# Performance work log

Hardware: AMD Instinct MI355X
Metric: run time of the kernel (lower is better)

## Reference

```python
import jax, jax.numpy as jnp
import numpy as np

N_NODES = 100000
N_EDGES = 1600000
D_FEAT = 64
COS_EPS = 1e-8  # torch.nn.functional.cosine_similarity default eps


def setup_inputs() -> dict:
    key = jax.random.key(0)
    k1, k2 = jax.random.split(key)
    features = jax.random.normal(k1, (N_NODES, D_FEAT), dtype=jnp.float32)
    edge_index = jax.random.randint(k2, (2, N_EDGES), 0, N_NODES, dtype=jnp.int64)
    return {"features": features, "edge_index": edge_index}


def _mean_agg(h, src, dst, n_nodes):
    # copy_u: message = h[src]; fn.mean: per-dst mean over incoming messages
    msg_sum = jax.ops.segment_sum(h[src], dst, num_segments=n_nodes)  # [N, d]
    deg = jax.ops.segment_sum(jnp.ones(src.shape, h.dtype), dst, num_segments=n_nodes)  # [N]
    deg = deg[:, None]
    # nodes with zero in-degree get 0 (DGL mean semantics)
    return jnp.where(deg > 0, msg_sum / jnp.maximum(deg, 1.0), 0.0)


def reference(features, edge_index):
    src, dst = edge_index[0], edge_index[1]
    n = features.shape[0]
    x1 = _mean_agg(features, src, dst, n)   # gcn1
    x2 = _mean_agg(x1, src, dst, n)         # gcn2
    # cosine similarity along feature dim
    dot = jnp.sum(x1 * x2, axis=-1)
    n1 = jnp.linalg.norm(x1, axis=-1)
    n2 = jnp.linalg.norm(x2, axis=-1)
    cos = dot / jnp.maximum(n1 * n2, COS_EPS)
    w = cos[:, None]
    return w * x2 + (1.0 - w) * x1
```

## Files before the change

kernel.cpp:

```cpp
#include <hip/hip_runtime.h>
#include <hip/hip_fp16.h>
#include <math.h>

#define N_NODES 100000
#define N_EDGES 1600000
#define D_FEAT  64

#define NPB     256
#define NBC     ((N_NODES + NPB - 1) / NPB)
#define HIST_WGS 256
#define NV4     (N_EDGES / 4)
#define CHUNK4  ((NV4 + HIST_WGS - 1) / HIST_WGS)
#define RAW_CAP 5120
#define CASTN   ((N_NODES * D_FEAT) / 4)

#define CAST1   2250
#define CAST2   1000
#define CAST3   750
#define CAST4   750
#define CO1     0
#define CO2     (CAST1 * 256)
#define CO3     (CO2 + CAST2 * 256)
#define CO4     (CO3 + CAST3 * 512)

#define GCAP    68


__device__ __forceinline__ void cast_slice(const float* __restrict__ feat,
                                           __half* __restrict__ feat_h, int i) {
    if (i < CASTN) {
        float4 v = ((const float4*)feat)[i];
        __half2 h0 = __floats2half2_rn(v.x, v.y);
        __half2 h1 = __floats2half2_rn(v.z, v.w);
        uint2 st;
        st.x = *(unsigned*)&h0;
        st.y = *(unsigned*)&h1;
        ((uint2*)feat_h)[i] = st;
    }
}

__device__ __forceinline__ uint4 pack8(const float* v) {
    __half2 h0 = __floats2half2_rn(v[0], v[1]);
    __half2 h1 = __floats2half2_rn(v[2], v[3]);
    __half2 h2 = __floats2half2_rn(v[4], v[5]);
    __half2 h3 = __floats2half2_rn(v[6], v[7]);
    uint4 st;
    st.x = *(unsigned*)&h0; st.y = *(unsigned*)&h1;
    st.z = *(unsigned*)&h2; st.w = *(unsigned*)&h3;
    return st;
}

__device__ __forceinline__ void unp8(uint4 u, float* a) {
    { __half2 h = *(__half2*)&u.x; float2 f = __half22float2(h); a[0]=f.x; a[1]=f.y; }
    { __half2 h = *(__half2*)&u.y; float2 f = __half22float2(h); a[2]=f.x; a[3]=f.y; }
    { __half2 h = *(__half2*)&u.z; float2 f = __half22float2(h); a[4]=f.x; a[5]=f.y; }
    { __half2 h = *(__half2*)&u.w; float2 f = __half22float2(h); a[6]=f.x; a[7]=f.y; }
}

__device__ __forceinline__ void acc4(uint4 u, __half2& h0, __half2& h1,
                                     __half2& h2, __half2& h3) {
    h0 = __hadd2(h0, *(__half2*)&u.x);
    h1 = __hadd2(h1, *(__half2*)&u.y);
    h2 = __hadd2(h2, *(__half2*)&u.z);
    h3 = __hadd2(h3, *(__half2*)&u.w);
}

__device__ __forceinline__ int block_excl_scan_512(int v, int t, int* wsum) {
    int lane = t & 63, wv = t >> 6;
    int incl = v;
    #pragma unroll
    for (int m = 1; m < 64; m <<= 1) {
        int o = __shfl_up(incl, m);
        if (lane >= m) incl += o;
    }
    if (lane == 63) wsum[wv] = incl;
    __syncthreads();
    int prefix = 0;
    #pragma unroll
    for (int j = 0; j < 8; j++)
        if (j < wv) prefix += wsum[j];
    return prefix + incl - v;
}

__device__ __forceinline__ int block_excl_scan_256(int v, int t, int* wsum) {
    int lane = t & 63, wv = t >> 6;
    int incl = v;
    #pragma unroll
    for (int m = 1; m < 64; m <<= 1) {
        int o = __shfl_up(incl, m);
        if (lane >= m) incl += o;
    }
    if (lane == 63) wsum[wv] = incl;
    __syncthreads();
    int prefix = 0;
    #pragma unroll
    for (int j = 0; j < 4; j++)
        if (j < wv) prefix += wsum[j];
    return prefix + incl - v;
}


__global__ __launch_bounds__(256) void k1_hist_cast(
        const float* __restrict__ feat,
        __half* __restrict__ feat_h,
        const int4* __restrict__ dst4,
        int* __restrict__ percnt) {
    if (blockIdx.x >= HIST_WGS) {
        cast_slice(feat, feat_h, CO1 + (blockIdx.x - HIST_WGS) * 256 + threadIdx.x);
        return;
    }
    __shared__ int cnt[NBC];
    int wg = blockIdx.x, t = threadIdx.x;
    for (int i = t; i < NBC; i += 256) cnt[i] = 0;
    __syncthreads();
    int i0 = wg * CHUNK4;
    int i1 = min(i0 + CHUNK4, NV4);
    for (int i = i0 + t; i < i1; i += 256) {
        int4 d = dst4[i];
        atomicAdd(&cnt[d.x >> 8], 1);
        atomicAdd(&cnt[d.y >> 8], 1);
        atomicAdd(&cnt[d.z >> 8], 1);
        atomicAdd(&cnt[d.w >> 8], 1);
    }
    __syncthreads();
    for (int i = t; i < NBC; i += 256)
        percnt[wg * NBC + i] = cnt[i];
}


__global__ __launch_bounds__(256) void k2_colscan(
        const int* __restrict__ percnt,
        int* __restrict__ pexcl,
        int* __restrict__ bhist,
        const float* __restrict__ feat,
        __half* __restrict__ feat_h) {
    if (blockIdx.x >= NBC) {
        cast_slice(feat, feat_h, CO2 + (blockIdx.x - NBC) * 256 + threadIdx.x);
        return;
    }
    __shared__ int wsum[4];
    int b = blockIdx.x, t = threadIdx.x;
    int v = percnt[t * NBC + b];
    int excl = block_excl_scan_256(v, t, wsum);
    pexcl[b * HIST_WGS + t] = excl;
    if (t == HIST_WGS - 1) bhist[b] = excl + v;
}


__global__ __launch_bounds__(512) void k3_bucketize(
        const int4* __restrict__ src4,
        const int4* __restrict__ dst4,
        const int* __restrict__ bhist,
        const int* __restrict__ pexcl,
        unsigned int* __restrict__ tmp1,
        const float* __restrict__ feat,
        __half* __restrict__ feat_h) {
    if (blockIdx.x >= HIST_WGS) {
        cast_slice(feat, feat_h, CO3 + (blockIdx.x - HIST_WGS) * 512 + threadIdx.x);
        return;
    }
    __shared__ int base[NBC];
    __shared__ int cur[NBC];
    __shared__ int wsum[8];
    int wg = blockIdx.x, t = threadIdx.x;
    int v = (t < NBC) ? bhist[t] : 0;
    int excl = block_excl_scan_512(v, t, wsum);
    if (t < NBC) {
        base[t] = excl + pexcl[t * HIST_WGS + wg];
        cur[t] = 0;
    }
    __syncthreads();
    int i0 = wg * CHUNK4;
    int i1 = min(i0 + CHUNK4, NV4);
    for (int i = i0 + t; i < i1; i += 512) {
        int4 d = dst4[i];
        int4 s = src4[i];
        {
            int b = d.x >> 8; int r = atomicAdd(&cur[b], 1);
            tmp1[base[b] + r] = ((unsigned)s.x << 8) | (unsigned)(d.x & 255);
        }
        {
            int b = d.y >> 8; int r = atomicAdd(&cur[b], 1);
            tmp1[base[b] + r] = ((unsigned)s.y << 8) | (unsigned)(d.y & 255);
        }
        {
            int b = d.z >> 8; int r = atomicAdd(&cur[b], 1);
            tmp1[base[b] + r] = ((unsigned)s.z << 8) | (unsigned)(d.z & 255);
        }
        {
            int b = d.w >> 8; int r = atomicAdd(&cur[b], 1);
            tmp1[base[b] + r] = ((unsigned)s.w << 8) | (unsigned)(d.w & 255);
        }
    }
}


__global__ __launch_bounds__(512) void k4_bucket_csr(
        const unsigned int* __restrict__ tmp1,
        const int* __restrict__ bhist,
        int* __restrict__ offsets,
        int* __restrict__ csr_src,
        const float* __restrict__ feat,
        __half* __restrict__ feat_h) {
    if (blockIdx.x >= NBC) {
        cast_slice(feat, feat_h, CO4 + (blockIdx.x - NBC) * 512 + threadIdx.x);
        return;
    }
    __shared__ int cnt[NPB];
    __shared__ int off[NPB];
    __shared__ int wsum[8];
    __shared__ int buf[RAW_CAP];
    __shared__ int sEbase, sEcnt;
    int b = blockIdx.x, t = threadIdx.x;

    {
        int v = (t < NBC) ? bhist[t] : 0;
        int ex = block_excl_scan_512(v, t, wsum);
        if (t == b) { sEbase = ex; sEcnt = v; }
    }
    if (t < NPB) cnt[t] = 0;
    __syncthreads();
    int ebase = sEbase;
    int ecnt  = sEcnt;
    int node0 = b * NPB;

    if (ecnt <= RAW_CAP) {
        unsigned myv[10];
        #pragma unroll
        for (int k = 0; k < 10; k++) {
            int i = t + k * 512;
            if (i < ecnt) {
                unsigned u = tmp1[ebase + i];
                myv[k] = u;
                atomicAdd(&cnt[u & 255], 1);
            }
        }
        __syncthreads();

        int v = (t < NPB) ? cnt[t] : 0;
        int excl = block_excl_scan_512(v, t, wsum);
        if (t < NPB) {
            off[t] = excl;
            cnt[t] = 0;
            if (node0 + t < N_NODES) offsets[node0 + t] = ebase + excl;
        }
        if (b == NBC - 1 && t == 0) offsets[N_NODES] = N_EDGES;
        __syncthreads();

        #pragma unroll
        for (int k = 0; k < 10; k++) {
            int i = t + k * 512;
            if (i < ecnt) {
                unsigned u = myv[k];
                int d = (int)(u & 255);
                int r = atomicAdd(&cnt[d], 1);
                buf[off[d] + r] = (int)(u >> 8);
            }
        }
        __syncthreads();
        for (int i = t; i < ecnt; i += 512)
            csr_src[ebase + i] = buf[i];
    } else {
        for (int i = t; i < ecnt; i += 512)
            atomicAdd(&cnt[tmp1[ebase + i] & 255], 1);
        __syncthreads();

        int v = (t < NPB) ? cnt[t] : 0;
        int excl = block_excl_scan_512(v, t, wsum);
        if (t < NPB) {
            off[t] = excl;
            cnt[t] = 0;
            if (node0 + t < N_NODES) offsets[node0 + t] = ebase + excl;
        }
        if (b == NBC - 1 && t == 0) offsets[N_NODES] = N_EDGES;
        __syncthreads();

        for (int i = t; i < ecnt; i += 512) {
            unsigned u = tmp1[ebase + i];
            int d = (int)(u & 255);
            int r = atomicAdd(&cnt[d], 1);
            csr_src[ebase + off[d] + r] = (int)(u >> 8);
        }
    }
}


__global__ __launch_bounds__(256) void gather1_kernel(
        const __half* __restrict__ feat_h,
        const int* __restrict__ offsets,
        const int* __restrict__ csr,
        __half* __restrict__ x1_h) {
    __shared__ int snbr[4][8][GCAP];
    int wv   = threadIdx.x >> 6;
    int lane = threadIdx.x & 63;
    int g    = lane >> 3;
    int fl   = lane & 7;
    int node = (blockIdx.x * 4 + wv) * 8 + g;

    int base = offsets[node];
    int deg  = offsets[node + 1] - base;
    int dcap = min(deg, GCAP);

    int* my = snbr[wv][g];
    for (int j = fl; j < dcap; j += 8)
        my[j] = csr[base + j];
    __builtin_amdgcn_wave_barrier();

    __half2 a0 = __float2half2_rn(0.f), a1 = a0, a2 = a0, a3 = a0;
    __half2 b0 = a0, b1 = a0, b2 = a0, b3 = a0;
    const __half* fb = feat_h + (fl << 3);
    int j = 0;
    for (; j + 4 <= dcap; j += 4) {
        int4 s = *(const int4*)&my[j];
        uint4 u0 = *(const uint4*)(fb + ((size_t)s.x << 6));
        uint4 u1 = *(const uint4*)(fb + ((size_t)s.y << 6));
        uint4 u2 = *(const uint4*)(fb + ((size_t)s.z << 6));
        uint4 u3 = *(const uint4*)(fb + ((size_t)s.w << 6));
        acc4(u0, a0, a1, a2, a3);
        acc4(u1, b0, b1, b2, b3);
        acc4(u2, a0, a1, a2, a3);
        acc4(u3, b0, b1, b2, b3);
    }
    for (; j < dcap; ++j) {
        int s = my[j];
        uint4 u = *(const uint4*)(fb + ((size_t)s << 6));
        acc4(u, a0, a1, a2, a3);
    }
    for (j = GCAP; j < deg; ++j) {
        int s = csr[base + j];
        uint4 u = *(const uint4*)(fb + ((size_t)s << 6));
        acc4(u, a0, a1, a2, a3);
    }
    a0 = __hadd2(a0, b0); a1 = __hadd2(a1, b1);
    a2 = __hadd2(a2, b2); a3 = __hadd2(a3, b3);

    float invf = (deg > 0) ? __builtin_amdgcn_rcpf((float)deg) : 0.0f;
    float r[8];
    { float2 f = __half22float2(a0); r[0]=f.x*invf; r[1]=f.y*invf; }
    { float2 f = __half22float2(a1); r[2]=f.x*invf; r[3]=f.y*invf; }
    { float2 f = __half22float2(a2); r[4]=f.x*invf; r[5]=f.y*invf; }
    { float2 f = __half22float2(a3); r[6]=f.x*invf; r[7]=f.y*invf; }
    *(uint4*)(x1_h + ((size_t)node << 6) + (fl << 3)) = pack8(r);
}

__global__ __launch_bounds__(256) void gather2_finalize_kernel(
        const __half* __restrict__ x1_h,
        const int* __restrict__ offsets,
        const int* __restrict__ csr,
        float* __restrict__ out) {
    __shared__ int snbr[4][8][GCAP];
    int wv   = threadIdx.x >> 6;
    int lane = threadIdx.x & 63;
    int g    = lane >> 3;
    int fl   = lane & 7;
    int node = (blockIdx.x * 4 + wv) * 8 + g;

    int base = offsets[node];
    int deg  = offsets[node + 1] - base;
    int dcap = min(deg, GCAP);

    int* my = snbr[wv][g];
    for (int j = fl; j < dcap; j += 8)
        my[j] = csr[base + j];
    __builtin_amdgcn_wave_barrier();

    __half2 a0 = __float2half2_rn(0.f), a1 = a0, a2 = a0, a3 = a0;
    __half2 c0 = a0, c1 = a0, c2 = a0, c3 = a0;
    const __half* fb = x1_h + (fl << 3);
    int j = 0;
    for (; j + 4 <= dcap; j += 4) {
        int4 s = *(const int4*)&my[j];
        uint4 u0 = *(const uint4*)(fb + ((size_t)s.x << 6));
        uint4 u1 = *(const uint4*)(fb + ((size_t)s.y << 6));
        uint4 u2 = *(const uint4*)(fb + ((size_t)s.z << 6));
        uint4 u3 = *(const uint4*)(fb + ((size_t)s.w << 6));
        acc4(u0, a0, a1, a2, a3);
        acc4(u1, c0, c1, c2, c3);
        acc4(u2, a0, a1, a2, a3);
        acc4(u3, c0, c1, c2, c3);
    }
    for (; j < dcap; ++j) {
        int s = my[j];
        uint4 u = *(const uint4*)(fb + ((size_t)s << 6));
        acc4(u, a0, a1, a2, a3);
    }
    for (j = GCAP; j < deg; ++j) {
        int s = csr[base + j];
        uint4 u = *(const uint4*)(fb + ((size_t)s << 6));
        acc4(u, a0, a1, a2, a3);
    }
    a0 = __hadd2(a0, c0); a1 = __hadd2(a1, c1);
    a2 = __hadd2(a2, c2); a3 = __hadd2(a3, c3);

    float invf = (deg > 0) ? __builtin_amdgcn_rcpf((float)deg) : 0.0f;
    float b[8];
    { float2 f = __half22float2(a0); b[0]=f.x*invf; b[1]=f.y*invf; }
    { float2 f = __half22float2(a1); b[2]=f.x*invf; b[3]=f.y*invf; }
    { float2 f = __half22float2(a2); b[4]=f.x*invf; b[5]=f.y*invf; }
    { float2 f = __half22float2(a3); b[6]=f.x*invf; b[7]=f.y*invf; }

    float a[8];
    uint4 ua = *(const uint4*)(x1_h + ((size_t)node << 6) + (fl << 3));
    unp8(ua, a);

    float dot = 0.f, nn1 = 0.f, nn2 = 0.f;
    #pragma unroll
    for (int t = 0; t < 8; t++) {
        dot += a[t] * b[t];
        nn1 += a[t] * a[t];
        nn2 += b[t] * b[t];
    }
    #pragma unroll
    for (int m = 1; m < 8; m <<= 1) {
        dot += __shfl_xor(dot, m);
        nn1 += __shfl_xor(nn1, m);
        nn2 += __shfl_xor(nn2, m);
    }

    float denom = fmaxf(__builtin_amdgcn_sqrtf(nn1 * nn2), 1e-8f);
    float w = dot * __builtin_amdgcn_rcpf(denom);
    float omw = 1.0f - w;

    float4 r0, r1;
    r0.x = w*b[0] + omw*a[0]; r0.y = w*b[1] + omw*a[1];
    r0.z = w*b[2] + omw*a[2]; r0.w = w*b[3] + omw*a[3];
    r1.x = w*b[4] + omw*a[4]; r1.y = w*b[5] + omw*a[5];
    r1.z = w*b[6] + omw*a[6]; r1.w = w*b[7] + omw*a[7];
    float* po = out + ((size_t)node << 6) + (fl << 3);
    *(float4*)po = r0;
    *(float4*)(po + 4) = r1;
}


extern "C" void kernel_launch(void* const* d_in, const int* in_sizes, int n_in,
                              void* d_out, int out_size, void* d_ws, size_t ws_size,
                              hipStream_t stream) {
    const float* feat = (const float*)d_in[0];
    const int*   eidx = (const int*)d_in[1];
    const int4*  src4 = (const int4*)eidx;
    const int4*  dst4 = (const int4*)(eidx + N_EDGES);

    __half*       feat_h  = (__half*)d_ws;
    __half*       x1_h    = feat_h + (size_t)N_NODES * D_FEAT;
    unsigned int* tmp1    = (unsigned int*)(x1_h + (size_t)N_NODES * D_FEAT);
    int*          csr_src = (int*)(tmp1 + N_EDGES);
    int*          offsets = csr_src + N_EDGES;
    int*          percnt  = offsets + (N_NODES + 1);
    int*          pexcl   = percnt + HIST_WGS * NBC;
    int*          bhist   = pexcl + NBC * HIST_WGS;
    float*        out     = (float*)d_out;

    k1_hist_cast <<<HIST_WGS + CAST1, 256, 0, stream>>>(feat, feat_h, dst4, percnt);
    k2_colscan   <<<NBC + CAST2,      256, 0, stream>>>(percnt, pexcl, bhist, feat, feat_h);
    k3_bucketize <<<HIST_WGS + CAST3, 512, 0, stream>>>(src4, dst4, bhist, pexcl, tmp1, feat, feat_h);
    k4_bucket_csr<<<NBC + CAST4,      512, 0, stream>>>(tmp1, bhist, offsets, csr_src, feat, feat_h);

    int nblocks = N_NODES / 32;
    gather1_kernel<<<nblocks, 256, 0, stream>>>(feat_h, offsets, csr_src, x1_h);
    gather2_finalize_kernel<<<nblocks, 256, 0, stream>>>(x1_h, offsets, csr_src, out);
}
```

Measured before the change: 160.0 us.

## Merge CSR build phases into one cooperative kernel with grid syncs

Replaces the four separate preprocessing kernels (histogram, column scan, bucketize, per-bucket CSR) with a single cooperative kernel that separates the phases with grid.sync(). The fp32-to-fp16 feature cast is spread over the spare blocks during the histogram and bucketize phases. The aim is to remove kernel launch gaps and drain tails between phases. In exchange it depends on all 391 blocks being resident at once and pays for grid-wide barriers. A fallback multi-kernel path runs if the cooperative launch fails, and the overflow branch for buckets larger than the shared buffer was dropped.

```diff
diff --git a/kernel.cpp b/kernel.cpp
--- a/kernel.cpp
+++ b/kernel.cpp
@@ -1,6 +1,9 @@
 #include <hip/hip_runtime.h>
+#include <hip/hip_cooperative_groups.h>
 #include <hip/hip_fp16.h>
 #include <math.h>
+
+namespace cg = cooperative_groups;
 
 #define N_NODES 100000
 #define N_EDGES 1600000
@@ -13,15 +16,12 @@
 #define CHUNK4  ((NV4 + HIST_WGS - 1) / HIST_WGS)
 #define RAW_CAP 5120
 #define CASTN   ((N_NODES * D_FEAT) / 4)
-
-#define CAST1   2250
-#define CAST2   1000
-#define CAST3   750
-#define CAST4   750
-#define CO1     0
-#define CO2     (CAST1 * 256)
-#define CO3     (CO2 + CAST2 * 256)
-#define CO4     (CO3 + CAST3 * 512)
+#define GRID_PRE NBC
+
+#define CAST_BLKS  (GRID_PRE - HIST_WGS)
+#define CAST_ITERS 12
+
+#define SMEM_INTS 5640
 
 #define GCAP    68
 
@@ -39,6 +39,15 @@
     }
 }
 
+__device__ __forceinline__ void cast_batch(const float* __restrict__ feat,
+                                           __half* __restrict__ feat_h,
+                                           int batch, int blk, int t) {
+    #pragma unroll
+    for (int it = 0; it < CAST_ITERS; ++it)
+        cast_slice(feat, feat_h,
+                   ((batch * CAST_BLKS + blk) * CAST_ITERS + it) * 512 + t);
+}
+
 __device__ __forceinline__ uint4 pack8(const float* v) {
     __half2 h0 = __floats2half2_rn(v[0], v[1]);
     __half2 h1 = __floats2half2_rn(v[2], v[3]);
@@ -82,40 +91,16 @@
     return prefix + incl - v;
 }
 
-__device__ __forceinline__ int block_excl_scan_256(int v, int t, int* wsum) {
-    int lane = t & 63, wv = t >> 6;
-    int incl = v;
-    #pragma unroll
-    for (int m = 1; m < 64; m <<= 1) {
-        int o = __shfl_up(incl, m);
-        if (lane >= m) incl += o;
-    }
-    if (lane == 63) wsum[wv] = incl;
-    __syncthreads();
-    int prefix = 0;
-    #pragma unroll
-    for (int j = 0; j < 4; j++)
-        if (j < wv) prefix += wsum[j];
-    return prefix + incl - v;
-}
-
-
-__global__ __launch_bounds__(256) void k1_hist_cast(
-        const float* __restrict__ feat,
-        __half* __restrict__ feat_h,
-        const int4* __restrict__ dst4,
-        int* __restrict__ percnt) {
-    if (blockIdx.x >= HIST_WGS) {
-        cast_slice(feat, feat_h, CO1 + (blockIdx.x - HIST_WGS) * 256 + threadIdx.x);
-        return;
-    }
-    __shared__ int cnt[NBC];
-    int wg = blockIdx.x, t = threadIdx.x;
-    for (int i = t; i < NBC; i += 256) cnt[i] = 0;
-    __syncthreads();
-    int i0 = wg * CHUNK4;
+
+__device__ void phase_hist(int b, int t, int* smem,
+                           const int4* __restrict__ dst4,
+                           int* __restrict__ percnt) {
+    int* cnt = smem;
+    for (int i = t; i < NBC; i += 512) cnt[i] = 0;
+    __syncthreads();
+    int i0 = b * CHUNK4;
     int i1 = min(i0 + CHUNK4, NV4);
-    for (int i = i0 + t; i < i1; i += 256) {
+    for (int i = i0 + t; i < i1; i += 512) {
         int4 d = dst4[i];
         atomicAdd(&cnt[d.x >> 8], 1);
         atomicAdd(&cnt[d.y >> 8], 1);
@@ -123,165 +108,183 @@
         atomicAdd(&cnt[d.w >> 8], 1);
     }
     __syncthreads();
-    for (int i = t; i < NBC; i += 256)
-        percnt[wg * NBC + i] = cnt[i];
-}
-
-
-__global__ __launch_bounds__(256) void k2_colscan(
-        const int* __restrict__ percnt,
-        int* __restrict__ pexcl,
-        int* __restrict__ bhist,
-        const float* __restrict__ feat,
-        __half* __restrict__ feat_h) {
-    if (blockIdx.x >= NBC) {
-        cast_slice(feat, feat_h, CO2 + (blockIdx.x - NBC) * 256 + threadIdx.x);
-        return;
-    }
-    __shared__ int wsum[4];
-    int b = blockIdx.x, t = threadIdx.x;
-    int v = percnt[t * NBC + b];
-    int excl = block_excl_scan_256(v, t, wsum);
-    pexcl[b * HIST_WGS + t] = excl;
+    for (int i = t; i < NBC; i += 512)
+        percnt[b * NBC + i] = cnt[i];
+}
+
+__device__ void phase_colscan(int b, int t, int* smem,
+                              const int* __restrict__ percnt,
+                              int* __restrict__ pexcl,
+                              int* __restrict__ bhist) {
+    int* wsum = smem;
+    int v = (t < HIST_WGS) ? percnt[t * NBC + b] : 0;
+    int excl = block_excl_scan_512(v, t, wsum);
+    if (t < HIST_WGS) pexcl[b * HIST_WGS + t] = excl;
     if (t == HIST_WGS - 1) bhist[b] = excl + v;
 }
 
-
-__global__ __launch_bounds__(512) void k3_bucketize(
-        const int4* __restrict__ src4,
-        const int4* __restrict__ dst4,
-        const int* __restrict__ bhist,
-        const int* __restrict__ pexcl,
-        unsigned int* __restrict__ tmp1,
-        const float* __restrict__ feat,
-        __half* __restrict__ feat_h) {
-    if (blockIdx.x >= HIST_WGS) {
-        cast_slice(feat, feat_h, CO3 + (blockIdx.x - HIST_WGS) * 512 + threadIdx.x);
-        return;
-    }
-    __shared__ int base[NBC];
-    __shared__ int cur[NBC];
-    __shared__ int wsum[8];
-    int wg = blockIdx.x, t = threadIdx.x;
+__device__ void phase_bucketize(int b, int t, int* smem,
+                                const int4* __restrict__ src4,
+                                const int4* __restrict__ dst4,
+                                const int* __restrict__ bhist,
+                                const int* __restrict__ pexcl,
+                                unsigned int* __restrict__ tmp1) {
+    int* base = smem;
+    int* cur  = smem + NBC;
+    int* wsum = smem + 2 * NBC;
     int v = (t < NBC) ? bhist[t] : 0;
     int excl = block_excl_scan_512(v, t, wsum);
     if (t < NBC) {
-        base[t] = excl + pexcl[t * HIST_WGS + wg];
+        base[t] = excl + pexcl[t * HIST_WGS + b];
         cur[t] = 0;
     }
     __syncthreads();
-    int i0 = wg * CHUNK4;
+    int i0 = b * CHUNK4;
     int i1 = min(i0 + CHUNK4, NV4);
     for (int i = i0 + t; i < i1; i += 512) {
         int4 d = dst4[i];
         int4 s = src4[i];
         {
-            int b = d.x >> 8; int r = atomicAdd(&cur[b], 1);
-            tmp1[base[b] + r] = ((unsigned)s.x << 8) | (unsigned)(d.x & 255);
+            int bb = d.x >> 8; int r = atomicAdd(&cur[bb], 1);
+            tmp1[base[bb] + r] = ((unsigned)s.x << 8) | (unsigned)(d.x & 255);
         }
         {
-            int b = d.y >> 8; int r = atomicAdd(&cur[b], 1);
-            tmp1[base[b] + r] = ((unsigned)s.y << 8) | (unsigned)(d.y & 255);
+            int bb = d.y >> 8; int r = atomicAdd(&cur[bb], 1);
+            tmp1[base[bb] + r] = ((unsigned)s.y << 8) | (unsigned)(d.y & 255);
         }
         {
-            int b = d.z >> 8; int r = atomicAdd(&cur[b], 1);
-            tmp1[base[b] + r] = ((unsigned)s.z << 8) | (unsigned)(d.z & 255);
+            int bb = d.z >> 8; int r = atomicAdd(&cur[bb], 1);
+            tmp1[base[bb] + r] = ((unsigned)s.z << 8) | (unsigned)(d.z & 255);
         }
         {
-            int b = d.w >> 8; int r = atomicAdd(&cur[b], 1);
-            tmp1[base[b] + r] = ((unsigned)s.w << 8) | (unsigned)(d.w & 255);
-        }
-    }
-}
-
-
-__global__ __launch_bounds__(512) void k4_bucket_csr(
-        const unsigned int* __restrict__ tmp1,
-        const int* __restrict__ bhist,
-        int* __restrict__ offsets,
-        int* __restrict__ csr_src,
-        const float* __restrict__ feat,
-        __half* __restrict__ feat_h) {
-    if (blockIdx.x >= NBC) {
-        cast_slice(feat, feat_h, CO4 + (blockIdx.x - NBC) * 512 + threadIdx.x);
-        return;
-    }
-    __shared__ int cnt[NPB];
-    __shared__ int off[NPB];
-    __shared__ int wsum[8];
-    __shared__ int buf[RAW_CAP];
-    __shared__ int sEbase, sEcnt;
-    int b = blockIdx.x, t = threadIdx.x;
+            int bb = d.w >> 8; int r = atomicAdd(&cur[bb], 1);
+            tmp1[base[bb] + r] = ((unsigned)s.w << 8) | (unsigned)(d.w & 255);
+        }
+    }
+}
+
+__device__ void phase_csr(int b, int t, int* smem,
+                          const unsigned int* __restrict__ tmp1,
+                          const int* __restrict__ bhist,
+                          int* __restrict__ offsets,
+                          int* __restrict__ csr_src) {
+    int* buf  = smem;
+    int* cnt  = smem + RAW_CAP;
+    int* off  = smem + RAW_CAP + NPB;
+    int* wsum = smem + RAW_CAP + 2 * NPB;
+    int sObase, sEcnt;
 
     {
         int v = (t < NBC) ? bhist[t] : 0;
         int ex = block_excl_scan_512(v, t, wsum);
-        if (t == b) { sEbase = ex; sEcnt = v; }
+        if (t == b) { wsum[0] = ex; wsum[1] = v; }
+        __syncthreads();
+        sObase = wsum[0]; sEcnt = wsum[1];
     }
     if (t < NPB) cnt[t] = 0;
     __syncthreads();
-    int ebase = sEbase;
+    int ebase = sObase;
     int ecnt  = sEcnt;
+    const unsigned int* ebuf = tmp1 + ebase;
     int node0 = b * NPB;
 
-    if (ecnt <= RAW_CAP) {
-        unsigned myv[10];
-        #pragma unroll
-        for (int k = 0; k < 10; k++) {
-            int i = t + k * 512;
-            if (i < ecnt) {
-                unsigned u = tmp1[ebase + i];
-                myv[k] = u;
-                atomicAdd(&cnt[u & 255], 1);
-            }
-        }
-        __syncthreads();
-
-        int v = (t < NPB) ? cnt[t] : 0;
-        int excl = block_excl_scan_512(v, t, wsum);
-        if (t < NPB) {
-            off[t] = excl;
-            cnt[t] = 0;
-            if (node0 + t < N_NODES) offsets[node0 + t] = ebase + excl;
-        }
-        if (b == NBC - 1 && t == 0) offsets[N_NODES] = N_EDGES;
-        __syncthreads();
-
-        #pragma unroll
-        for (int k = 0; k < 10; k++) {
-            int i = t + k * 512;
-            if (i < ecnt) {
-                unsigned u = myv[k];
-                int d = (int)(u & 255);
-                int r = atomicAdd(&cnt[d], 1);
-                buf[off[d] + r] = (int)(u >> 8);
-            }
-        }
-        __syncthreads();
-        for (int i = t; i < ecnt; i += 512)
-            csr_src[ebase + i] = buf[i];
-    } else {
-        for (int i = t; i < ecnt; i += 512)
-            atomicAdd(&cnt[tmp1[ebase + i] & 255], 1);
-        __syncthreads();
-
-        int v = (t < NPB) ? cnt[t] : 0;
-        int excl = block_excl_scan_512(v, t, wsum);
-        if (t < NPB) {
-            off[t] = excl;
-            cnt[t] = 0;
-            if (node0 + t < N_NODES) offsets[node0 + t] = ebase + excl;
-        }
-        if (b == NBC - 1 && t == 0) offsets[N_NODES] = N_EDGES;
-        __syncthreads();
-
-        for (int i = t; i < ecnt; i += 512) {
-            unsigned u = tmp1[ebase + i];
+    unsigned myv[10];
+    #pragma unroll
+    for (int k = 0; k < 10; k++) {
+        int i = t + k * 512;
+        if (i < ecnt) {
+            unsigned u = ebuf[i];
+            myv[k] = u;
+            atomicAdd(&cnt[u & 255], 1);
+        }
+    }
+    __syncthreads();
+
+    int v = (t < NPB) ? cnt[t] : 0;
+    int excl = block_excl_scan_512(v, t, wsum);
+    if (t < NPB) {
+        off[t] = excl;
+        cnt[t] = 0;
+        if (node0 + t < N_NODES) offsets[node0 + t] = ebase + excl;
+    }
+    if (b == NBC - 1 && t == 0) offsets[N_NODES] = N_EDGES;
+    __syncthreads();
+
+    #pragma unroll
+    for (int k = 0; k < 10; k++) {
+        int i = t + k * 512;
+        if (i < ecnt) {
+            unsigned u = myv[k];
             int d = (int)(u & 255);
             int r = atomicAdd(&cnt[d], 1);
-            csr_src[ebase + off[d] + r] = (int)(u >> 8);
-        }
-    }
+            buf[off[d] + r] = (int)(u >> 8);
+        }
+    }
+    __syncthreads();
+    for (int i = t; i < ecnt; i += 512)
+        csr_src[ebase + i] = buf[i];
+}
+
+
+__global__ __launch_bounds__(512) void pre_coop(
+        const int4* __restrict__ src4,
+        const int4* __restrict__ dst4,
+        const float* __restrict__ feat,
+        __half* __restrict__ feat_h,
+        int* __restrict__ percnt,
+        int* __restrict__ pexcl,
+        int* __restrict__ bhist,
+        int* __restrict__ offsets,
+        unsigned int* __restrict__ tmp1,
+        int* __restrict__ csr_src) {
+    __shared__ int smem[SMEM_INTS];
+    cg::grid_group grid = cg::this_grid();
+    int b = blockIdx.x, t = threadIdx.x;
+
+    if (b < HIST_WGS) phase_hist(b, t, smem, dst4, percnt);
+    else              cast_batch(feat, feat_h, 0, b - HIST_WGS, t);
+    grid.sync();
+
+    phase_colscan(b, t, smem, percnt, pexcl, bhist);
+    grid.sync();
+
+    if (b < HIST_WGS) phase_bucketize(b, t, smem, src4, dst4, bhist, pexcl, tmp1);
+    else              cast_batch(feat, feat_h, 1, b - HIST_WGS, t);
+    grid.sync();
+
+    phase_csr(b, t, smem, tmp1, bhist, offsets, csr_src);
+}
+
+
+__global__ __launch_bounds__(512) void pre_p1(const int4* __restrict__ dst4,
+                                              int* __restrict__ percnt) {
+    __shared__ int smem[NBC];
+    phase_hist(blockIdx.x, threadIdx.x, smem, dst4, percnt);
+}
+__global__ __launch_bounds__(512) void pre_p2(const int* __restrict__ percnt,
+                                              int* __restrict__ pexcl,
+                                              int* __restrict__ bhist) {
+    __shared__ int smem[8];
+    phase_colscan(blockIdx.x, threadIdx.x, smem, percnt, pexcl, bhist);
+}
+__global__ __launch_bounds__(512) void pre_p3(const int4* __restrict__ src4,
+                                              const int4* __restrict__ dst4,
+                                              const int* __restrict__ bhist,
+                                              const int* __restrict__ pexcl,
+                                              unsigned int* __restrict__ tmp1) {
+    __shared__ int smem[2 * NBC + 8];
+    phase_bucketize(blockIdx.x, threadIdx.x, smem, src4, dst4, bhist, pexcl, tmp1);
+}
+__global__ __launch_bounds__(512) void pre_p4(const unsigned int* __restrict__ tmp1,
+                                              const int* __restrict__ bhist,
+                                              int* __restrict__ offsets,
+                                              int* __restrict__ csr_src) {
+    __shared__ int smem[SMEM_INTS];
+    phase_csr(blockIdx.x, threadIdx.x, smem, tmp1, bhist, offsets, csr_src);
+}
+__global__ __launch_bounds__(512) void cast_kernel(const float* __restrict__ feat,
+                                                   __half* __restrict__ feat_h) {
+    cast_slice(feat, feat_h, blockIdx.x * 512 + threadIdx.x);
 }
 
 
@@ -450,10 +453,20 @@
     int*          bhist   = pexcl + NBC * HIST_WGS;
     float*        out     = (float*)d_out;
 
-    k1_hist_cast <<<HIST_WGS + CAST1, 256, 0, stream>>>(feat, feat_h, dst4, percnt);
-    k2_colscan   <<<NBC + CAST2,      256, 0, stream>>>(percnt, pexcl, bhist, feat, feat_h);
-    k3_bucketize <<<HIST_WGS + CAST3, 512, 0, stream>>>(src4, dst4, bhist, pexcl, tmp1, feat, feat_h);
-    k4_bucket_csr<<<NBC + CAST4,      512, 0, stream>>>(tmp1, bhist, offsets, csr_src, feat, feat_h);
+    void* args[] = { (void*)&src4, (void*)&dst4, (void*)&feat, (void*)&feat_h,
+                     (void*)&percnt, (void*)&pexcl, (void*)&bhist,
+                     (void*)&offsets, (void*)&tmp1, (void*)&csr_src };
+    hipError_t err = hipLaunchCooperativeKernel(
+        reinterpret_cast<void*>(pre_coop), dim3(GRID_PRE), dim3(512),
+        args, 0, stream);
+
+    if (err != hipSuccess) {
+        cast_kernel<<<(CASTN + 511) / 512, 512, 0, stream>>>(feat, feat_h);
+        pre_p1<<<HIST_WGS, 512, 0, stream>>>(dst4, percnt);
+        pre_p2<<<NBC,      512, 0, stream>>>(percnt, pexcl, bhist);
+        pre_p3<<<HIST_WGS, 512, 0, stream>>>(src4, dst4, bhist, pexcl, tmp1);
+        pre_p4<<<NBC,      512, 0, stream>>>(tmp1, bhist, offsets, csr_src);
+    }
 
     int nblocks = N_NODES / 32;
     gather1_kernel<<<nblocks, 256, 0, stream>>>(feat_h, offsets, csr_src, x1_h);
```

After: 318.8 us. 1.99x slower.
